# Performance work log

Hardware: AMD Instinct MI355X
Metric: run time of the kernel (lower is better)

The kernel has to match this reference:

```python
import jax, jax.numpy as jnp
import numpy as np

B, T, D = 4, 2048, 1024


def ste_sign(x):
    # forward: sign(x); backward: identity (straight-through)
    return jax.lax.stop_gradient(jnp.sign(x) - x) + x


def setup_inputs() -> dict:
    key = jax.random.key(0)
    kx, kq, kk, kv = jax.random.split(key, 4)
    return {
        "x": jax.random.normal(kx, (B, T, D), dtype=jnp.float32),
        "bv_q": jax.random.normal(kq, (D,), dtype=jnp.float32) * 0.02,
        "bv_k": jax.random.normal(kk, (D,), dtype=jnp.float32) * 0.02,
        "bv_v": jax.random.normal(kv, (D,), dtype=jnp.float32) * 0.02,
    }


def reference(x, bv_q, bv_k, bv_v):
    d = x.shape[-1]
    scale = d ** (-0.5)
    bq = ste_sign(bv_q)
    bk = ste_sign(bv_k)
    bv = ste_sign(bv_v)
    Q = ste_sign(x * bq)          # [B,T,D], values in {-1,0,1}
    K = ste_sign(x * bk)
    V = x * bv                    # [B,T,D]
    scores = jnp.einsum('btd,bsd->bts', Q, K) * scale  # [B,T,T]
    t = x.shape[1]
    causal = jnp.tril(jnp.ones((t, t), dtype=bool))    # [T,T]
    scores = jnp.where(causal, scores, -jnp.inf)
    attn = jax.nn.sigmoid(scores * 4.0)
    attn = jnp.where(causal, attn, 0.0)
    return jnp.einsum('bts,bsd->btd', attn, V)
```

## Files before the change

kernel.cpp:

```cpp
#include <hip/hip_runtime.h>
#include <hip/hip_bf16.h>
#include <stdint.h>
#include <math.h>

#define B_SZ 4
#define T_SZ 2048
#define D_SZ 1024

constexpr int NTH = 512;

typedef short bf16x8 __attribute__((ext_vector_type(8)));
typedef float f32x4 __attribute__((ext_vector_type(4)));
typedef int i32x4 __attribute__((ext_vector_type(4)));
typedef unsigned short ushort8 __attribute__((ext_vector_type(8)));

__device__ __forceinline__ uint32_t sbf(uint32_t xu, uint32_t su) {
  return 0x3F80u | (((xu ^ su) >> 16) & 0x8000u);
}

__device__ __forceinline__ ushort f2bf(float f) {
  uint32_t u = __float_as_uint(f);
  return (ushort)((u + 0x7FFFu + ((u >> 16) & 1u)) >> 16);
}

__device__ __forceinline__ void glds16(const void* g, void* l) {
  __builtin_amdgcn_global_load_lds(
      (const __attribute__((address_space(1))) void*)g,
      (__attribute__((address_space(3))) void*)l, 16, 0, 0);
}


__global__ __launch_bounds__(256) void prep_kernel(
    const float* __restrict__ x, const float* __restrict__ bvq,
    const float* __restrict__ bvk, const float* __restrict__ bvv,
    char* __restrict__ Qb, char* __restrict__ Kb, ushort* __restrict__ Vt2) {
  __shared__ ushort vt[64][72];
  const int bid = blockIdx.x;
  const int dt = bid & 15;
  const int tt = (bid >> 4) & 31;
  const int b = bid >> 9;
  const int t0 = tt * 64, d0 = dt * 64;
  const int tid = threadIdx.x;

#pragma unroll
  for (int p = 0; p < 4; ++p) {
    const int row = p * 16 + (tid >> 4);
    const int c4 = tid & 15;
    const size_t idx = ((size_t)(b * T_SZ + t0 + row)) * D_SZ + d0 + c4 * 4;
    float4 v = *(const float4*)(x + idx);
    float4 q = *(const float4*)(bvq + d0 + c4 * 4);
    float4 k = *(const float4*)(bvk + d0 + c4 * 4);
    float4 s = *(const float4*)(bvv + d0 + c4 * 4);
    uint32_t xu[4] = {__float_as_uint(v.x), __float_as_uint(v.y),
                      __float_as_uint(v.z), __float_as_uint(v.w)};
    uint32_t qu[4] = {__float_as_uint(q.x), __float_as_uint(q.y),
                      __float_as_uint(q.z), __float_as_uint(q.w)};
    uint32_t ku[4] = {__float_as_uint(k.x), __float_as_uint(k.y),
                      __float_as_uint(k.z), __float_as_uint(k.w)};
    uint32_t su[4] = {__float_as_uint(s.x), __float_as_uint(s.y),
                      __float_as_uint(s.z), __float_as_uint(s.w)};
    uint32_t qw = 0, kw = 0;
#pragma unroll
    for (int j = 0; j < 4; ++j) {
      uint32_t qb = ((xu[j] ^ qu[j]) & 0x80000000u) ? 0xFFu : 0x01u;
      uint32_t kb = ((xu[j] ^ ku[j]) & 0x80000000u) ? 0xFFu : 0x01u;
      qw |= qb << (8 * j);
      kw |= kb << (8 * j);
      vt[row][c4 * 4 + j] = f2bf(__uint_as_float(xu[j] ^ (su[j] & 0x80000000u)));
    }
    *(uint32_t*)(Qb + idx) = qw;
    *(uint32_t*)(Kb + idx) = kw;
  }
  __syncthreads();
#pragma unroll
  for (int p = 0; p < 2; ++p) {
    const int dr = p * 32 + (tid >> 3);
    const int tc = tid & 7;
    ushort8 o;
#pragma unroll
    for (int j = 0; j < 8; ++j) o[j] = vt[tc * 8 + j][dr];
    const int dglob = d0 + dr;
    const int s8 = (t0 >> 3) + tc;
    *(ushort8*)(Vt2 +
                (((size_t)(b * 64 + (dglob >> 4))) * 256 + s8) * 128 +
                (dglob & 15) * 8) = o;
  }
}

__global__ __launch_bounds__(NTH) void score_kernel(
    const char* __restrict__ Qb, const char* __restrict__ Kb,
    ushort* __restrict__ P2) {
  __shared__ __align__(16) unsigned char Qs[2][128 * 128];
  __shared__ __align__(16) unsigned char Ks[2][128 * 128];

  const int bid = blockIdx.x;
  const int xcd = bid & 7;
  const int b = xcd >> 1;
  const int j = ((bid >> 3) << 1) + (xcd & 1);
  int qt = (int)((sqrtf(8.f * (float)j + 1.f) - 1.f) * 0.5f);
  while ((qt + 1) * (qt + 2) / 2 <= j) ++qt;
  while (qt * (qt + 1) / 2 > j) --qt;
  const int st = j - qt * (qt + 1) / 2;

  const int tid = threadIdx.x;
  const int lane = tid & 63, w = tid >> 6;
  const int wr = w >> 1, wc = w & 1;
  const int l15 = lane & 15, l4 = lane >> 4;

  const size_t qrow0 = ((size_t)(b * T_SZ + qt * 128)) * D_SZ;
  const size_t krow0 = ((size_t)(b * T_SZ + st * 128)) * D_SZ;

  i32x4 sacc[2][4];
#pragma unroll
  for (int mf = 0; mf < 2; ++mf)
#pragma unroll
    for (int nf = 0; nf < 4; ++nf) sacc[mf][nf] = (i32x4){0, 0, 0, 0};

  auto STAGE = [&](int buf, int ks) {
#pragma unroll
    for (int i = 0; i < 4; ++i) {
      const int isK = i >> 1;
      const int fi = tid + (i & 1) * 512;
      const int row = fi >> 3, c = fi & 7;
      const int cs = c ^ (row & 7);
      const char* src = (isK ? Kb + krow0 : Qb + qrow0) +
                        (size_t)row * D_SZ + ks * 128 + cs * 16;
      unsigned char* dst = (isK ? Ks[buf] : Qs[buf]) + fi * 16;
      glds16(src, dst);
    }
  };

  STAGE(0, 0);
  for (int ks = 0; ks < 8; ++ks) {
    asm volatile("s_waitcnt vmcnt(0)" ::: "memory");
    __builtin_amdgcn_s_barrier();
    if (ks + 1 < 8) STAGE((ks + 1) & 1, ks + 1);
    const int buf = ks & 1;
#pragma unroll
    for (int kc = 0; kc < 2; ++kc) {
      i32x4 af[2], bfr[4];
#pragma unroll
      for (int mf = 0; mf < 2; ++mf) {
        const int row = wr * 32 + mf * 16 + l15;
        const int ch = (kc * 4 + l4) ^ (row & 7);
        af[mf] = *(const i32x4*)(Qs[buf] + row * 128 + ch * 16);
      }
#pragma unroll
      for (int nf = 0; nf < 4; ++nf) {
        const int row = wc * 64 + nf * 16 + l15;
        const int ch = (kc * 4 + l4) ^ (row & 7);
        bfr[nf] = *(const i32x4*)(Ks[buf] + row * 128 + ch * 16);
      }
#pragma unroll
      for (int mf = 0; mf < 2; ++mf)
#pragma unroll
        for (int nf = 0; nf < 4; ++nf)
          sacc[mf][nf] = __builtin_amdgcn_mfma_i32_16x16x64_i8(
              af[mf], bfr[nf], sacc[mf][nf], 0, 0, 0);
    }
    asm volatile("s_waitcnt lgkmcnt(0)" ::: "memory");
  }

#pragma unroll
  for (int mf = 0; mf < 2; ++mf)
#pragma unroll
    for (int nf = 0; nf < 4; ++nf)
#pragma unroll
      for (int r = 0; r < 4; ++r) {
        const int qg = qt * 128 + wr * 32 + mf * 16 + l4 * 4 + r;
        const int sg = st * 128 + wc * 64 + nf * 16 + l15;
        float p = 1.f / (1.f + __expf(-0.125f * (float)sacc[mf][nf][r]));
        if (sg > qg) p = 0.f;
        P2[(((size_t)(b * 128 + (qg >> 4))) * 256 + (sg >> 3)) * 128 +
           (qg & 15) * 8 + (sg & 7)] = f2bf(p);
      }
}

__global__ __launch_bounds__(256) void pv_kernel(
    const ushort* __restrict__ P2, const ushort* __restrict__ Vt2,
    float* __restrict__ out) {
  const int bid = blockIdx.x;
  const int xcd = bid & 7;
  const int idx = bid >> 3;
  const int ds = idx & 7;
  const int prh = idx >> 3;
  const int pr = prh * 2 + (xcd & 1);
  const int b = xcd >> 1;

  const int tid = threadIdx.x;
  const int lane = tid & 63, w = tid >> 6;
  const int wr = w >> 1, dg = w & 1;
  const int l15 = lane & 15, l4 = lane >> 4;

  const size_t d4base = (size_t)b * 64 + ds * 8 + dg * 4;

  for (int half = 0; half < 2; ++half) {
    const int qt = half ? (31 - pr) : pr;

    f32x4 acc[2][4];
#pragma unroll
    for (int mf = 0; mf < 2; ++mf)
#pragma unroll
      for (int nf = 0; nf < 4; ++nf) acc[mf][nf] = (f32x4){0.f, 0.f, 0.f, 0.f};

    const size_t q4base = (size_t)b * 128 + qt * 4 + wr * 2;

    const ushort* pP0 = P2 + ((q4base + 0) * 256 + l4) * 128 + l15 * 8;
    const ushort* pP1 = P2 + ((q4base + 1) * 256 + l4) * 128 + l15 * 8;
    const ushort* pV0 = Vt2 + ((d4base + 0) * 256 + l4) * 128 + l15 * 8;
    const ushort* pV1 = Vt2 + ((d4base + 1) * 256 + l4) * 128 + l15 * 8;
    const ushort* pV2 = Vt2 + ((d4base + 2) * 256 + l4) * 128 + l15 * 8;
    const ushort* pV3 = Vt2 + ((d4base + 3) * 256 + l4) * 128 + l15 * 8;

    const int nk = (qt + 1) * 2;
#pragma unroll 2
    for (int k = 0; k < nk; ++k) {
      bf16x8 pa0 = *(const bf16x8*)pP0;
      bf16x8 pa1 = *(const bf16x8*)pP1;
      bf16x8 vb0 = *(const bf16x8*)pV0;
      bf16x8 vb1 = *(const bf16x8*)pV1;
      bf16x8 vb2 = *(const bf16x8*)pV2;
      bf16x8 vb3 = *(const bf16x8*)pV3;
      pP0 += 512; pP1 += 512;
      pV0 += 512; pV1 += 512; pV2 += 512; pV3 += 512;
      acc[0][0] = __builtin_amdgcn_mfma_f32_16x16x32_bf16(pa0, vb0, acc[0][0], 0, 0, 0);
      acc[0][1] = __builtin_amdgcn_mfma_f32_16x16x32_bf16(pa0, vb1, acc[0][1], 0, 0, 0);
      acc[0][2] = __builtin_amdgcn_mfma_f32_16x16x32_bf16(pa0, vb2, acc[0][2], 0, 0, 0);
      acc[0][3] = __builtin_amdgcn_mfma_f32_16x16x32_bf16(pa0, vb3, acc[0][3], 0, 0, 0);
      acc[1][0] = __builtin_amdgcn_mfma_f32_16x16x32_bf16(pa1, vb0, acc[1][0], 0, 0, 0);
      acc[1][1] = __builtin_amdgcn_mfma_f32_16x16x32_bf16(pa1, vb1, acc[1][1], 0, 0, 0);
      acc[1][2] = __builtin_amdgcn_mfma_f32_16x16x32_bf16(pa1, vb2, acc[1][2], 0, 0, 0);
      acc[1][3] = __builtin_amdgcn_mfma_f32_16x16x32_bf16(pa1, vb3, acc[1][3], 0, 0, 0);
    }

    float* ob = out + ((size_t)(b * T_SZ + qt * 64 + wr * 32)) * D_SZ +
                ds * 128 + dg * 64;
#pragma unroll
    for (int mf = 0; mf < 2; ++mf)
#pragma unroll
      for (int nf = 0; nf < 4; ++nf)
#pragma unroll
        for (int r = 0; r < 4; ++r)
          ob[(size_t)(mf * 16 + l4 * 4 + r) * D_SZ + nf * 16 + l15] =
              acc[mf][nf][r];
  }
}

__global__ __launch_bounds__(NTH) void hdc_attn_fallback(
    const float* __restrict__ x, const float* __restrict__ bvq,
    const float* __restrict__ bvk, const float* __restrict__ bvv,
    float* __restrict__ out) {
  __shared__ ushort Qs[32][1032];
  __shared__ ushort Ks[64][72];
  __shared__ ushort Ps[32][72];
  const int tid = threadIdx.x;
  const int lane = tid & 63;
  const int w = tid >> 6;
  const int rg = w >> 2, cg = w & 3;
  const int l15 = lane & 15, l4 = lane >> 4;
  const int b = blockIdx.x >> 6;
  const int ti = blockIdx.x & 63;
  const int t0 = ti * 32;
  {
    const float4* xr = (const float4*)(x + ((size_t)b * T_SZ + t0) * D_SZ);
    const float4* bq4 = (const float4*)bvq;
#pragma unroll
    for (int i = 0; i < 16; ++i) {
      int flat4 = tid + i * NTH;
      int row = flat4 >> 8, c4 = flat4 & 255;
      float4 v = xr[row * 256 + c4];
      float4 q = bq4[c4];
      uint32_t q0 = sbf(__float_as_uint(v.x), __float_as_uint(q.x));
      uint32_t q1 = sbf(__float_as_uint(v.y), __float_as_uint(q.y));
      uint32_t q2 = sbf(__float_as_uint(v.z), __float_as_uint(q.z));
      uint32_t q3 = sbf(__float_as_uint(v.w), __float_as_uint(q.w));
      *(uint2*)&Qs[row][c4 * 4] = make_uint2(q0 | (q1 << 16), q2 | (q3 << 16));
    }
  }
  uint32_t vsign[16];
#pragma unroll
  for (int f = 0; f < 16; ++f)
    vsign[f] = __float_as_uint(bvv[cg * 256 + f * 16 + l15]) & 0x80000000u;
  f32x4 acc[16];
#pragma unroll
  for (int f = 0; f < 16; ++f) acc[f] = (f32x4){0.f, 0.f, 0.f, 0.f};
  const int nt = (t0 + 32 + 63) / 64;
  for (int st = 0; st < nt; ++st) {
    const int s0 = st * 64;
    f32x4 sacc = (f32x4){0.f, 0.f, 0.f, 0.f};
    for (int dc = 0; dc < D_SZ / 64; ++dc) {
      __syncthreads();
      {
        const int s = tid >> 3;
        const int c8 = (tid & 7) * 8;
        const float* xk = x + ((size_t)b * T_SZ + s0 + s) * D_SZ + dc * 64 + c8;
        const float* bk = bvk + dc * 64 + c8;
        float4 v0 = *(const float4*)xk;
        float4 v1 = *(const float4*)(xk + 4);
        float4 k0 = *(const float4*)bk;
        float4 k1 = *(const float4*)(bk + 4);
        uint32_t w0 = sbf(__float_as_uint(v0.x), __float_as_uint(k0.x)) |
                      (sbf(__float_as_uint(v0.y), __float_as_uint(k0.y)) << 16);
        uint32_t w1 = sbf(__float_as_uint(v0.z), __float_as_uint(k0.z)) |
                      (sbf(__float_as_uint(v0.w), __float_as_uint(k0.w)) << 16);
        uint32_t w2 = sbf(__float_as_uint(v1.x), __float_as_uint(k1.x)) |
                      (sbf(__float_as_uint(v1.y), __float_as_uint(k1.y)) << 16);
        uint32_t w3 = sbf(__float_as_uint(v1.z), __float_as_uint(k1.z)) |
                      (sbf(__float_as_uint(v1.w), __float_as_uint(k1.w)) << 16);
        *(uint4*)&Ks[s][c8] = make_uint4(w0, w1, w2, w3);
      }
      __syncthreads();
#pragma unroll
      for (int h = 0; h < 2; ++h) {
        bf16x8 a = *(const bf16x8*)&Qs[rg * 16 + l15][dc * 64 + h * 32 + l4 * 8];
        bf16x8 kb = *(const bf16x8*)&Ks[cg * 16 + l15][h * 32 + l4 * 8];
        sacc = __builtin_amdgcn_mfma_f32_16x16x32_bf16(a, kb, sacc, 0, 0, 0);
      }
    }
    {
      const int scol = cg * 16 + l15;
      const int sg = s0 + scol;
#pragma unroll
      for (int r = 0; r < 4; ++r) {
        const int m = rg * 16 + l4 * 4 + r;
        float p = 0.f;
        if (sg <= t0 + m) p = 1.f / (1.f + __expf(-0.125f * sacc[r]));
        Ps[m][scol] = (ushort)(__float_as_uint(p) >> 16);
      }
    }
    __syncthreads();
    const float* xv = x + ((size_t)b * T_SZ + s0) * D_SZ;
#pragma unroll
    for (int kk = 0; kk < 2; ++kk) {
      bf16x8 pa = *(const bf16x8*)&Ps[rg * 16 + l15][kk * 32 + l4 * 8];
      const float* xvs = xv + (size_t)(kk * 32 + l4 * 8) * D_SZ;
#pragma unroll
      for (int f = 0; f < 16; ++f) {
        const int n = cg * 256 + f * 16 + l15;
        const float* xn = xvs + n;
        bf16x8 vb;
#pragma unroll
        for (int i = 0; i < 8; ++i) {
          uint32_t u = __float_as_uint(xn[(size_t)i * D_SZ]) ^ vsign[f];
          vb[i] = (short)(u >> 16);
        }
        acc[f] = __builtin_amdgcn_mfma_f32_16x16x32_bf16(pa, vb, acc[f], 0, 0, 0);
      }
    }
  }
  float* orow = out + ((size_t)b * T_SZ + t0) * D_SZ;
#pragma unroll
  for (int f = 0; f < 16; ++f) {
    const int n = cg * 256 + f * 16 + l15;
#pragma unroll
    for (int r = 0; r < 4; ++r) {
      const int m = rg * 16 + l4 * 4 + r;
      orow[(size_t)m * D_SZ + n] = acc[f][r];
    }
  }
}

extern "C" void kernel_launch(void* const* d_in, const int* in_sizes, int n_in,
                              void* d_out, int out_size, void* d_ws, size_t ws_size,
                              hipStream_t stream) {
  const float* x = (const float*)d_in[0];
  const float* bvq = (const float*)d_in[1];
  const float* bvk = (const float*)d_in[2];
  const float* bvv = (const float*)d_in[3];
  float* out = (float*)d_out;

  const size_t QB_SZ = (size_t)B_SZ * T_SZ * D_SZ;
  const size_t VT_SZ = QB_SZ * 2;
  const size_t P_SZ = (size_t)B_SZ * T_SZ * T_SZ * 2;
  const size_t NEED_FULL = QB_SZ * 2 + VT_SZ + P_SZ;

  if (ws_size >= NEED_FULL) {
    char* Qb = (char*)d_ws;
    char* Kb = Qb + QB_SZ;
    ushort* Vt2 = (ushort*)(Kb + QB_SZ);
    ushort* P2 = (ushort*)((char*)Vt2 + VT_SZ);
    hipLaunchKernelGGL(prep_kernel, dim3(B_SZ * 32 * 16), dim3(256), 0, stream,
                       x, bvq, bvk, bvv, Qb, Kb, Vt2);
    hipLaunchKernelGGL(score_kernel, dim3(544), dim3(NTH), 0, stream,
                       Qb, Kb, P2);
    hipLaunchKernelGGL(pv_kernel, dim3(512), dim3(256), 0, stream,
                       P2, Vt2, out);
  } else {
    hipLaunchKernelGGL(hdc_attn_fallback, dim3(B_SZ * 64), dim3(256), 0, stream,
                       x, bvq, bvk, bvv, out);
  }
}
```

Before: 70.01 us.

## Store Q/K in MFMA fragment layout and load directly without LDS staging

The prep kernel now writes the sign-binarized Q and K in a tiled fragment layout: 16-row tiles, each holding 16 chunks of 64 bytes per row, in the order the int8 MFMA expects. The score kernel reads its operand fragments straight from global memory into registers. This removes the LDS double buffering, the barriers and the waitcnt synchronization. In exchange, K fragments are re-read by several waves through the cache, and load latency is no longer hidden by explicit prefetching.

New measurement: 85.93 us. +22.8%, slower.

```diff
diff --git a/kernel.cpp b/kernel.cpp
--- a/kernel.cpp
+++ b/kernel.cpp
@@ -23,17 +23,11 @@
   return (ushort)((u + 0x7FFFu + ((u >> 16) & 1u)) >> 16);
 }
 
-__device__ __forceinline__ void glds16(const void* g, void* l) {
-  __builtin_amdgcn_global_load_lds(
-      (const __attribute__((address_space(1))) void*)g,
-      (__attribute__((address_space(3))) void*)l, 16, 0, 0);
-}
-
 
 __global__ __launch_bounds__(256) void prep_kernel(
     const float* __restrict__ x, const float* __restrict__ bvq,
     const float* __restrict__ bvk, const float* __restrict__ bvv,
-    char* __restrict__ Qb, char* __restrict__ Kb, ushort* __restrict__ Vt2) {
+    char* __restrict__ Qf, char* __restrict__ Kf, ushort* __restrict__ Vt2) {
   __shared__ ushort vt[64][72];
   const int bid = blockIdx.x;
   const int dt = bid & 15;
@@ -68,8 +62,12 @@
       kw |= kb << (8 * j);
       vt[row][c4 * 4 + j] = f2bf(__uint_as_float(xu[j] ^ (su[j] & 0x80000000u)));
     }
-    *(uint32_t*)(Qb + idx) = qw;
-    *(uint32_t*)(Kb + idx) = kw;
+    const int qg = t0 + row;
+    const size_t fo =
+        ((((size_t)(b * 128 + (qg >> 4))) * 16 + dt) * 16 + (qg & 15)) * 64 +
+        c4 * 4;
+    *(uint32_t*)(Qf + fo) = qw;
+    *(uint32_t*)(Kf + fo) = kw;
   }
   __syncthreads();
 #pragma unroll
@@ -88,11 +86,8 @@
 }
 
 __global__ __launch_bounds__(NTH) void score_kernel(
-    const char* __restrict__ Qb, const char* __restrict__ Kb,
+    const char* __restrict__ Qf, const char* __restrict__ Kf,
     ushort* __restrict__ P2) {
-  __shared__ __align__(16) unsigned char Qs[2][128 * 128];
-  __shared__ __align__(16) unsigned char Ks[2][128 * 128];
-
   const int bid = blockIdx.x;
   const int xcd = bid & 7;
   const int b = xcd >> 1;
@@ -107,58 +102,38 @@
   const int wr = w >> 1, wc = w & 1;
   const int l15 = lane & 15, l4 = lane >> 4;
 
-  const size_t qrow0 = ((size_t)(b * T_SZ + qt * 128)) * D_SZ;
-  const size_t krow0 = ((size_t)(b * T_SZ + st * 128)) * D_SZ;
-
   i32x4 sacc[2][4];
 #pragma unroll
   for (int mf = 0; mf < 2; ++mf)
 #pragma unroll
     for (int nf = 0; nf < 4; ++nf) sacc[mf][nf] = (i32x4){0, 0, 0, 0};
 
-  auto STAGE = [&](int buf, int ks) {
-#pragma unroll
-    for (int i = 0; i < 4; ++i) {
-      const int isK = i >> 1;
-      const int fi = tid + (i & 1) * 512;
-      const int row = fi >> 3, c = fi & 7;
-      const int cs = c ^ (row & 7);
-      const char* src = (isK ? Kb + krow0 : Qb + qrow0) +
-                        (size_t)row * D_SZ + ks * 128 + cs * 16;
-      unsigned char* dst = (isK ? Ks[buf] : Qs[buf]) + fi * 16;
-      glds16(src, dst);
-    }
-  };
-
-  STAGE(0, 0);
-  for (int ks = 0; ks < 8; ++ks) {
-    asm volatile("s_waitcnt vmcnt(0)" ::: "memory");
-    __builtin_amdgcn_s_barrier();
-    if (ks + 1 < 8) STAGE((ks + 1) & 1, ks + 1);
-    const int buf = ks & 1;
-#pragma unroll
-    for (int kc = 0; kc < 2; ++kc) {
-      i32x4 af[2], bfr[4];
-#pragma unroll
-      for (int mf = 0; mf < 2; ++mf) {
-        const int row = wr * 32 + mf * 16 + l15;
-        const int ch = (kc * 4 + l4) ^ (row & 7);
-        af[mf] = *(const i32x4*)(Qs[buf] + row * 128 + ch * 16);
-      }
-#pragma unroll
-      for (int nf = 0; nf < 4; ++nf) {
-        const int row = wc * 64 + nf * 16 + l15;
-        const int ch = (kc * 4 + l4) ^ (row & 7);
-        bfr[nf] = *(const i32x4*)(Ks[buf] + row * 128 + ch * 16);
-      }
-#pragma unroll
-      for (int mf = 0; mf < 2; ++mf)
-#pragma unroll
-        for (int nf = 0; nf < 4; ++nf)
-          sacc[mf][nf] = __builtin_amdgcn_mfma_i32_16x16x64_i8(
-              af[mf], bfr[nf], sacc[mf][nf], 0, 0, 0);
-    }
-    asm volatile("s_waitcnt lgkmcnt(0)" ::: "memory");
+  const int lo = l15 * 64 + l4 * 16;
+  const char* pQ0 = Qf + (((size_t)(b * 128 + qt * 8 + wr * 2 + 0)) << 14) + lo;
+  const char* pQ1 = Qf + (((size_t)(b * 128 + qt * 8 + wr * 2 + 1)) << 14) + lo;
+  const char* pK0 = Kf + (((size_t)(b * 128 + st * 8 + wc * 4 + 0)) << 14) + lo;
+  const char* pK1 = Kf + (((size_t)(b * 128 + st * 8 + wc * 4 + 1)) << 14) + lo;
+  const char* pK2 = Kf + (((size_t)(b * 128 + st * 8 + wc * 4 + 2)) << 14) + lo;
+  const char* pK3 = Kf + (((size_t)(b * 128 + st * 8 + wc * 4 + 3)) << 14) + lo;
+
+#pragma unroll 4
+  for (int kc = 0; kc < 16; ++kc) {
+    i32x4 a0 = *(const i32x4*)pQ0;
+    i32x4 a1 = *(const i32x4*)pQ1;
+    i32x4 b0 = *(const i32x4*)pK0;
+    i32x4 b1 = *(const i32x4*)pK1;
+    i32x4 b2 = *(const i32x4*)pK2;
+    i32x4 b3 = *(const i32x4*)pK3;
+    pQ0 += 1024; pQ1 += 1024;
+    pK0 += 1024; pK1 += 1024; pK2 += 1024; pK3 += 1024;
+    sacc[0][0] = __builtin_amdgcn_mfma_i32_16x16x64_i8(a0, b0, sacc[0][0], 0, 0, 0);
+    sacc[0][1] = __builtin_amdgcn_mfma_i32_16x16x64_i8(a0, b1, sacc[0][1], 0, 0, 0);
+    sacc[0][2] = __builtin_amdgcn_mfma_i32_16x16x64_i8(a0, b2, sacc[0][2], 0, 0, 0);
+    sacc[0][3] = __builtin_amdgcn_mfma_i32_16x16x64_i8(a0, b3, sacc[0][3], 0, 0, 0);
+    sacc[1][0] = __builtin_amdgcn_mfma_i32_16x16x64_i8(a1, b0, sacc[1][0], 0, 0, 0);
+    sacc[1][1] = __builtin_amdgcn_mfma_i32_16x16x64_i8(a1, b1, sacc[1][1], 0, 0, 0);
+    sacc[1][2] = __builtin_amdgcn_mfma_i32_16x16x64_i8(a1, b2, sacc[1][2], 0, 0, 0);
+    sacc[1][3] = __builtin_amdgcn_mfma_i32_16x16x64_i8(a1, b3, sacc[1][3], 0, 0, 0);
   }
 
 #pragma unroll
@@ -375,18 +350,18 @@
   const size_t NEED_FULL = QB_SZ * 2 + VT_SZ + P_SZ;
 
   if (ws_size >= NEED_FULL) {
-    char* Qb = (char*)d_ws;
-    char* Kb = Qb + QB_SZ;
-    ushort* Vt2 = (ushort*)(Kb + QB_SZ);
+    char* Qf = (char*)d_ws;
+    char* Kf = Qf + QB_SZ;
+    ushort* Vt2 = (ushort*)(Kf + QB_SZ);
     ushort* P2 = (ushort*)((char*)Vt2 + VT_SZ);
     hipLaunchKernelGGL(prep_kernel, dim3(B_SZ * 32 * 16), dim3(256), 0, stream,
-                       x, bvq, bvk, bvv, Qb, Kb, Vt2);
+                       x, bvq, bvk, bvv, Qf, Kf, Vt2);
     hipLaunchKernelGGL(score_kernel, dim3(544), dim3(NTH), 0, stream,
-                       Qb, Kb, P2);
+                       Qf, Kf, P2);
     hipLaunchKernelGGL(pv_kernel, dim3(512), dim3(256), 0, stream,
                        P2, Vt2, out);
   } else {
-    hipLaunchKernelGGL(hdc_attn_fallback, dim3(B_SZ * 64), dim3(256), 0, stream,
+    hipLaunchKernelGGL(hdc_attn_fallback, dim3(B_SZ * 64), dim3(NTH), 0, stream,
                        x, bvq, bvk, bvv, out);
   }
 }
```
